# Kernel tuning notes

Measured on AMD Instinct MI355X. Metric: run time of the kernel, lower is better.

## Reference

```python
import jax, jax.numpy as jnp
import numpy as np

N_NODES = 10000
N_EDGES = 160000
N_GRAPHS = 16
IN_FEAT = 128
DIMS = [(128, 512), (512, 256), (256, 64), (64, 32)]


def _lin_params(key, fin, fout):
    w = jax.random.normal(key, (fin, fout), jnp.float32) * (1.0 / np.sqrt(fin))
    b = jnp.zeros((fout,), jnp.float32)
    return w, b


def setup_inputs() -> dict:
    key = jax.random.key(0)
    ks = jax.random.split(key, 64)
    inp = {}
    inp['x'] = jax.random.normal(ks[0], (N_NODES, IN_FEAT), jnp.float32)
    inp['edge_index'] = jax.random.randint(ks[1], (2, N_EDGES), 0, N_NODES, jnp.int64 if jax.config.jax_enable_x64 else jnp.int32)
    inp['batch'] = jnp.sort(jax.random.randint(ks[2], (N_NODES,), 0, N_GRAPHS))
    ki = 3
    for li, (fin, fout) in enumerate(DIMS, start=1):
        for nm in ['q', 'k', 'v', 's']:
            w, b = _lin_params(ks[ki], fin, fout); ki += 1
            inp[f'W{nm}{li}'] = w
            inp[f'b{nm}{li}'] = b
    inp['Wg'], inp['bg'] = _lin_params(ks[ki], 32, 1); ki += 1
    inp['Wf'], inp['bf'] = _lin_params(ks[ki], 32, 9)
    return inp


def _segment_softmax(logits, seg, num_segments):
    m = jax.ops.segment_max(logits, seg, num_segments=num_segments)
    e = jnp.exp(logits - m[seg])
    s = jax.ops.segment_sum(e, seg, num_segments=num_segments)
    return e / s[seg]


def _transformer_conv(x, src, dst, Wq, bq, Wk, bk, Wv, bv, Ws, bs):
    # PyG TransformerConv, heads=1: attention over incoming edges per dst node.
    n = x.shape[0]
    q = x @ Wq + bq
    k = x @ Wk + bk
    v = x @ Wv + bv
    d = q.shape[-1]
    logits = jnp.sum(q[dst] * k[src], axis=-1) / jnp.sqrt(jnp.asarray(d, x.dtype))
    alpha = _segment_softmax(logits, dst, n)  # [E]
    agg = jax.ops.segment_sum(alpha[:, None] * v[src], dst, num_segments=n)
    return agg + (x @ Ws + bs)  # root/skip connection


def reference(x, edge_index, batch,
              Wq1, bq1, Wk1, bk1, Wv1, bv1, Ws1, bs1,
              Wq2, bq2, Wk2, bk2, Wv2, bv2, Ws2, bs2,
              Wq3, bq3, Wk3, bk3, Wv3, bv3, Ws3, bs3,
              Wq4, bq4, Wk4, bk4, Wv4, bv4, Ws4, bs4,
              Wg, bg, Wf, bf):
    src, dst = edge_index[0], edge_index[1]
    layers = [
        (Wq1, bq1, Wk1, bk1, Wv1, bv1, Ws1, bs1),
        (Wq2, bq2, Wk2, bk2, Wv2, bv2, Ws2, bs2),
        (Wq3, bq3, Wk3, bk3, Wv3, bv3, Ws3, bs3),
        (Wq4, bq4, Wk4, bk4, Wv4, bv4, Ws4, bs4),
    ]
    h = x
    for p in layers:
        h = jax.nn.elu(_transformer_conv(h, src, dst, *p))
    # GlobalAttention pooling: gate softmax per graph, weighted sum.
    gate = (h @ Wg + bg)[:, 0]  # [N]
    a = _segment_softmax(gate, batch, N_GRAPHS)
    pooled = jax.ops.segment_sum(a[:, None] * h, batch, num_segments=N_GRAPHS)  # [G, 32]
    return pooled @ Wf + bf  # [G, 9]
```

## Files before the change

kernel.cpp:

```cpp
#include <hip/hip_runtime.h>
#include <hip/hip_bf16.h>
#include <math.h>


typedef __bf16 bf16x8 __attribute__((ext_vector_type(8)));
typedef __bf16 bf16x4 __attribute__((ext_vector_type(4)));
typedef float f32x4 __attribute__((ext_vector_type(4)));

#define GBM 128
#define GBN 128
#define GBK 64

#if __has_builtin(__builtin_amdgcn_global_load_lds)
#define ASYNC_LDS 1
__device__ __forceinline__ void gload16(const __bf16* g, __bf16* l) {
  __builtin_amdgcn_global_load_lds(
      (const __attribute__((address_space(1))) unsigned int*)g,
      (__attribute__((address_space(3))) unsigned int*)l, 16, 0, 0);
}
#endif

__global__ __launch_bounds__(256) void gemm_mfma_kernel(
    const __bf16* __restrict__ A, const __bf16* __restrict__ Bt,
    const float* __restrict__ bias, __bf16* __restrict__ qkvs,
    int M, int K, int Nc) {
  __shared__ __bf16 As[GBM * 64];
  __shared__ __bf16 Bs[GBN * 64];
  const int tid = threadIdx.x;
  const int wave = tid >> 6;
  const int lane = tid & 63;
  const int quad = lane >> 4;
  const int l16 = lane & 15;
  const int m0 = blockIdx.y * GBM;
  const int n0 = blockIdx.x * GBN;
  const int wm = (wave & 1) * 64;
  const int wn = (wave >> 1) * 64;

  const int r8 = lane >> 3;
  const int sseg = lane & 7;

  f32x4 acc[4][4] = {};

  for (int k0 = 0; k0 < K; k0 += GBK) {
#pragma unroll
    for (int it = 0; it < 4; ++it) {
      const int rbase = wave * 32 + it * 8;
      const int row = rbase + r8;
      const int sw = sseg ^ r8;
      const __bf16* ga = A + (size_t)(m0 + row) * K + k0 + sw * 8;
      const __bf16* gb = Bt + (size_t)(n0 + row) * K + k0 + sw * 8;
#ifdef ASYNC_LDS
      gload16(ga, As + rbase * 64);
      gload16(gb, Bs + rbase * 64);
#else
      *(bf16x8*)(As + row * 64 + sseg * 8) = *(const bf16x8*)ga;
      *(bf16x8*)(Bs + row * 64 + sseg * 8) = *(const bf16x8*)gb;
#endif
    }
    __syncthreads();

#pragma unroll
    for (int ks = 0; ks < 2; ++ks) {
      bf16x8 af[4], bfr[4];
#pragma unroll
      for (int i = 0; i < 4; ++i) {
        const int ra = wm + i * 16 + l16;
        const int rb = wn + i * 16 + l16;
        const int ps = ((ks * 4 + quad) ^ (l16 & 7)) * 8;
        af[i]  = *(const bf16x8*)(As + ra * 64 + ps);
        bfr[i] = *(const bf16x8*)(Bs + rb * 64 + ps);
      }
#pragma unroll
      for (int mi = 0; mi < 4; ++mi)
#pragma unroll
        for (int ni = 0; ni < 4; ++ni)
          acc[mi][ni] = __builtin_amdgcn_mfma_f32_16x16x32_bf16(
              af[mi], bfr[ni], acc[mi][ni], 0, 0, 0);
    }
    __syncthreads();
  }

  float bsv[4];
#pragma unroll
  for (int ni = 0; ni < 4; ++ni) bsv[ni] = bias[n0 + wn + ni * 16 + l16];
#pragma unroll
  for (int mi = 0; mi < 4; ++mi) {
#pragma unroll
    for (int r = 0; r < 4; ++r) {
      int row = m0 + wm + mi * 16 + quad * 4 + r;
      if (row < M) {
        size_t rb = (size_t)row * Nc;
#pragma unroll
        for (int ni = 0; ni < 4; ++ni) {
          int col = n0 + wn + ni * 16 + l16;
          qkvs[rb + col] = (__bf16)(acc[mi][ni][r] + bsv[ni]);
        }
      }
    }
  }
}

#define WTOT 860160
#define BTOT 3456
#define XTOT 320000
__global__ void pack_all_kernel(
    const float* W0q, const float* W0k, const float* W0v, const float* W0s,
    const float* b0q, const float* b0k, const float* b0v, const float* b0s,
    const float* W1q, const float* W1k, const float* W1v, const float* W1s,
    const float* b1q, const float* b1k, const float* b1v, const float* b1s,
    const float* W2q, const float* W2k, const float* W2v, const float* W2s,
    const float* b2q, const float* b2k, const float* b2v, const float* b2s,
    const float* W3q, const float* W3k, const float* W3v, const float* W3s,
    const float* b3q, const float* b3k, const float* b3v, const float* b3s,
    const float* __restrict__ x, __bf16* __restrict__ xb,
    __bf16* __restrict__ Wt, float* __restrict__ bcat) {
  const int t = blockIdx.x * 256 + threadIdx.x;
  if (t < WTOT) {
    int l, local, ksh, fsh;
    if (t < 262144)      { l = 0; local = t;          ksh = 7; fsh = 9; }
    else if (t < 786432) { l = 1; local = t - 262144; ksh = 9; fsh = 8; }
    else if (t < 851968) { l = 2; local = t - 786432; ksh = 8; fsh = 6; }
    else                 { l = 3; local = t - 851968; ksh = 6; fsh = 5; }
    const int K = 1 << ksh, fout = 1 << fsh;
    int c = local >> ksh;
    int kk = local & (K - 1);
    int blk = c >> fsh;
    int j = c & (fout - 1);
    const float* W;
    if (l == 0)      W = blk == 0 ? W0q : blk == 1 ? W0k : blk == 2 ? W0v : W0s;
    else if (l == 1) W = blk == 0 ? W1q : blk == 1 ? W1k : blk == 2 ? W1v : W1s;
    else if (l == 2) W = blk == 0 ? W2q : blk == 1 ? W2k : blk == 2 ? W2v : W2s;
    else             W = blk == 0 ? W3q : blk == 1 ? W3k : blk == 2 ? W3v : W3s;
    Wt[t] = (__bf16)W[((size_t)kk << fsh) + j];
  } else if (t < WTOT + BTOT) {
    int u = t - WTOT;
    int l, local, fsh, boff;
    if (u < 2048)      { l = 0; local = u;        fsh = 9; boff = 0; }
    else if (u < 3072) { l = 1; local = u - 2048; fsh = 8; boff = 2048; }
    else if (u < 3328) { l = 2; local = u - 3072; fsh = 6; boff = 3072; }
    else               { l = 3; local = u - 3328; fsh = 5; boff = 3328; }
    const int fout = 1 << fsh;
    int blk = local >> fsh, j = local & (fout - 1);
    const float* b;
    if (l == 0)      b = blk == 0 ? b0q : blk == 1 ? b0k : blk == 2 ? b0v : b0s;
    else if (l == 1) b = blk == 0 ? b1q : blk == 1 ? b1k : blk == 2 ? b1v : b1s;
    else if (l == 2) b = blk == 0 ? b2q : blk == 1 ? b2k : blk == 2 ? b2v : b2s;
    else             b = blk == 0 ? b3q : blk == 1 ? b3k : blk == 2 ? b3v : b3s;
    bcat[boff + local] = b[j];
  } else if (t < WTOT + BTOT + XTOT) {
    int i = t - (WTOT + BTOT);
    float4 v = ((const float4*)x)[i];
    bf16x4 o;
    o[0] = (__bf16)v.x; o[1] = (__bf16)v.y; o[2] = (__bf16)v.z; o[3] = (__bf16)v.w;
    *(bf16x4*)(xb + (size_t)i * 4) = o;
  }
}

__global__ void hist_kernel(const int* __restrict__ dst, int* __restrict__ deg, int E) {
  int e = blockIdx.x * blockDim.x + threadIdx.x;
  if (e < E) atomicAdd(&deg[dst[e]], 1);
}

__global__ __launch_bounds__(1024) void scan_kernel(const int* __restrict__ deg,
                                                    int* __restrict__ offs, int N) {
  __shared__ int sums[1024];
  const int tid = threadIdx.x;
  const int chunk = (N + 1023) / 1024;
  const int start = tid * chunk;
  int s = 0;
  for (int i = 0; i < chunk; ++i) {
    int idx = start + i;
    if (idx < N) s += deg[idx];
  }
  sums[tid] = s;
  __syncthreads();
  for (int off = 1; off < 1024; off <<= 1) {
    int t = (tid >= off) ? sums[tid - off] : 0;
    __syncthreads();
    sums[tid] += t;
    __syncthreads();
  }
  int run = (tid == 0) ? 0 : sums[tid - 1];
  for (int i = 0; i < chunk; ++i) {
    int idx = start + i;
    if (idx < N) {
      offs[idx] = run;
      run += deg[idx];
    }
  }
  if (tid == 1023) offs[N] = sums[1023];
}

__global__ void scatter_kernel(const int* __restrict__ src, const int* __restrict__ dst,
                               const int* __restrict__ offs, int* __restrict__ cursor,
                               int* __restrict__ csr_src, int E) {
  int e = blockIdx.x * blockDim.x + threadIdx.x;
  if (e >= E) return;
  int d = dst[e];
  int pos = offs[d] + atomicAdd(&cursor[d], 1);
  csr_src[pos] = src[e];
}

template <int D, int LPG_LOG2, bool GATE>
__global__ __launch_bounds__(256) void attn_fused_kernel(
    const __bf16* __restrict__ qkvs, const int* __restrict__ csr_src,
    const int* __restrict__ offs, __bf16* __restrict__ h_out, int N,
    float scale, const float* __restrict__ Wg, const float* __restrict__ bg,
    float* __restrict__ gate_out) {
  constexpr int LPG = 1 << LPG_LOG2;
  constexpr int NG = 64 / LPG;
  constexpr int NIT = D / (8 * LPG);
  constexpr int LD = 4 * D;
  const int node = (blockIdx.x * 256 + threadIdx.x) >> 6;
  const int lane = threadIdx.x & 63;
  if (node >= N) return;
  const int g = lane >> LPG_LOG2;
  const int l = lane & (LPG - 1);
  const int begin = offs[node];
  const int deg = offs[node + 1] - begin;

  const __bf16* qrow = qkvs + (size_t)node * LD;
  bf16x8 qreg[NIT];
#pragma unroll
  for (int it = 0; it < NIT; ++it)
    qreg[it] = *(const bf16x8*)(qrow + it * LPG * 8 + l * 8);

  float m = -INFINITY;
  float s = 0.f;
  float acc[NIT][8] = {};

  for (int base = 0; base < deg; base += NG) {
    const int i = base + g;
    const bool valid = i < deg;
    int sidx = valid ? csr_src[begin + i] : 0;

    float p = 0.f;
    if (valid) {
      const __bf16* krow = qkvs + (size_t)sidx * LD + D;
      bf16x8 kv[NIT];
#pragma unroll
      for (int it = 0; it < NIT; ++it)
        kv[it] = *(const bf16x8*)(krow + it * LPG * 8 + l * 8);
#pragma unroll
      for (int it = 0; it < NIT; ++it)
#pragma unroll
        for (int j = 0; j < 8; ++j) p += (float)qreg[it][j] * (float)kv[it][j];
    }
#pragma unroll
    for (int off = LPG >> 1; off; off >>= 1) p += __shfl_xor(p, off);
    const float logit = valid ? p * scale : -INFINITY;

    float cmax = logit;
#pragma unroll
    for (int off = LPG; off < 64; off <<= 1)
      cmax = fmaxf(cmax, __shfl_xor(cmax, off));
    const float m_new = fmaxf(m, cmax);
    const float alpha = __expf(m - m_new);
    s *= alpha;
#pragma unroll
    for (int it = 0; it < NIT; ++it)
#pragma unroll
      for (int j = 0; j < 8; ++j) acc[it][j] *= alpha;
    const float w = __expf(logit - m_new);
    s += w;
    m = m_new;

    if (valid) {
      const __bf16* vrow = qkvs + (size_t)sidx * LD + 2 * D;
      bf16x8 vv[NIT];
#pragma unroll
      for (int it = 0; it < NIT; ++it)
        vv[it] = *(const bf16x8*)(vrow + it * LPG * 8 + l * 8);
#pragma unroll
      for (int it = 0; it < NIT; ++it)
#pragma unroll
        for (int j = 0; j < 8; ++j) acc[it][j] += w * (float)vv[it][j];
    }
  }

#pragma unroll
  for (int off = LPG; off < 64; off <<= 1) {
    s += __shfl_xor(s, off);
#pragma unroll
    for (int it = 0; it < NIT; ++it)
#pragma unroll
      for (int j = 0; j < 8; ++j) acc[it][j] += __shfl_xor(acc[it][j], off);
  }
  const float inv = (deg > 0) ? (1.0f / s) : 0.f;

  if (g == 0) {
    float rr[NIT][8];
#pragma unroll
    for (int it = 0; it < NIT; ++it) {
      const int f0 = it * LPG * 8 + l * 8;
      bf16x8 sk = *(const bf16x8*)(qrow + 3 * D + f0);
      bf16x8 o;
#pragma unroll
      for (int j = 0; j < 8; ++j) {
        float r = acc[it][j] * inv + (float)sk[j];
        r = (r > 0.f) ? r : expm1f(r);
        rr[it][j] = r;
        o[j] = (__bf16)r;
      }
      *(bf16x8*)(h_out + (size_t)node * D + f0) = o;
    }
    if (GATE) {
      float gp = 0.f;
#pragma unroll
      for (int j = 0; j < 8; ++j) gp += rr[0][j] * Wg[l * 8 + j];
#pragma unroll
      for (int off = 1; off < LPG; off <<= 1) gp += __shfl_xor(gp, off);
      if (l == 0) gate_out[node] = gp + bg[0];
    }
  }
}

__global__ __launch_bounds__(256) void pool_final_kernel(
    const __bf16* __restrict__ h, const float* __restrict__ gate,
    const int* __restrict__ batch, int N, const float* __restrict__ Wf,
    const float* __restrict__ bf_, float* __restrict__ out) {
  __shared__ float red[256];
  __shared__ float pooled_s[32];
  __shared__ float m_s, inv_s;
  __shared__ int sb[2];
  const int g = blockIdx.x;
  const int tid = threadIdx.x;

  if (tid < 2) {
    int target = g + tid;
    int lo = 0, hi = N;
    while (lo < hi) {
      int mid = (lo + hi) >> 1;
      if (batch[mid] < target) lo = mid + 1;
      else hi = mid;
    }
    sb[tid] = lo;
  }
  __syncthreads();
  const int s = sb[0];
  const int e_end = sb[1];

  float m = -INFINITY;
  for (int i = s + tid; i < e_end; i += 256) m = fmaxf(m, gate[i]);
  red[tid] = m;
  __syncthreads();
  for (int off = 128; off; off >>= 1) {
    if (tid < off) red[tid] = fmaxf(red[tid], red[tid + off]);
    __syncthreads();
  }
  if (tid == 0) m_s = red[0];
  __syncthreads();
  m = m_s;

  float ss = 0.f;
  for (int i = s + tid; i < e_end; i += 256) ss += __expf(gate[i] - m);
  red[tid] = ss;
  __syncthreads();
  for (int off = 128; off; off >>= 1) {
    if (tid < off) red[tid] += red[tid + off];
    __syncthreads();
  }
  if (tid == 0) inv_s = (e_end > s) ? (1.0f / red[0]) : 0.f;
  __syncthreads();
  const float inv = inv_s;

  const int f = tid & 31;
  const int grp = tid >> 5;
  float acc = 0.f;
  for (int i = s + grp; i < e_end; i += 8)
    acc += __expf(gate[i] - m) * (float)h[(size_t)i * 32 + f];
  red[tid] = acc;
  __syncthreads();
  if (tid < 32) {
    float a = 0.f;
#pragma unroll
    for (int j = 0; j < 8; ++j) a += red[j * 32 + tid];
    pooled_s[tid] = a * inv;
  }
  __syncthreads();

  if (tid < 9) {
    float o = bf_[tid];
#pragma unroll
    for (int kk = 0; kk < 32; ++kk) o += pooled_s[kk] * Wf[kk * 9 + tid];
    out[g * 9 + tid] = o;
  }
}

extern "C" void kernel_launch(void* const* d_in, const int* in_sizes, int n_in,
                              void* d_out, int out_size, void* d_ws, size_t ws_size,
                              hipStream_t stream) {
  const int N = in_sizes[2];
  const int E = in_sizes[1] / 2;
  const int G = 16;
  const int NP = N + 128;

  const float* x = (const float*)d_in[0];
  const int* ei = (const int*)d_in[1];
  const int* batch = (const int*)d_in[2];
  const int* src = ei;
  const int* dst = ei + E;
  const float* Wg = (const float*)d_in[35];
  const float* bg = (const float*)d_in[36];
  const float* Wf = (const float*)d_in[37];
  const float* bf_ = (const float*)d_in[38];
  float* out = (float*)d_out;

  char* p = (char*)d_ws;
  auto carve = [&](size_t bytes) -> char* {
    char* r = p;
    p += (bytes + 255) & ~(size_t)255;
    return r;
  };
  int* deg = (int*)carve((size_t)2 * N * 4);
  int* cursor = deg + N;
  int* offs = (int*)carve((size_t)(N + 1) * 4);
  int* csr_src = (int*)carve((size_t)E * 4);
  __bf16* Ab = (__bf16*)carve((size_t)NP * 128 * 2);
  __bf16* Wt = (__bf16*)carve((size_t)WTOT * 2);
  float* bcat = (float*)carve(BTOT * 4);
  __bf16* qkvs = (__bf16*)carve((size_t)N * 2048 * 2);
  __bf16* ha = (__bf16*)carve((size_t)NP * 512 * 2);
  __bf16* hb = (__bf16*)carve((size_t)NP * 512 * 2);
  float* gate = (float*)carve((size_t)N * 4);
  (void)ws_size;

  hipMemsetAsync(deg, 0, (size_t)2 * N * 4, stream);
  hist_kernel<<<(E + 255) / 256, 256, 0, stream>>>(dst, deg, E);
  scan_kernel<<<1, 1024, 0, stream>>>(deg, offs, N);
  scatter_kernel<<<(E + 255) / 256, 256, 0, stream>>>(src, dst, offs, cursor, csr_src, E);

  const float** di = (const float**)d_in;
  pack_all_kernel<<<(WTOT + BTOT + XTOT + 255) / 256, 256, 0, stream>>>(
      di[3], di[5], di[7], di[9], di[4], di[6], di[8], di[10],
      di[11], di[13], di[15], di[17], di[12], di[14], di[16], di[18],
      di[19], di[21], di[23], di[25], di[20], di[22], di[24], di[26],
      di[27], di[29], di[31], di[33], di[28], di[30], di[32], di[34],
      x, Ab, Wt, bcat);

  const int fins[4] = {128, 512, 256, 64};
  const int fouts[4] = {512, 256, 64, 32};
  const size_t woffs[4] = {0, 262144, 786432, 851968};
  const int boffs[4] = {0, 2048, 3072, 3328};
  const __bf16* hin = Ab;
  __bf16* houts[4] = {ha, hb, ha, hb};
  const int agrid = ((size_t)N * 64 + 255) / 256;

  for (int l = 0; l < 4; ++l) {
    const int fin = fins[l], fout = fouts[l];
    const int Nc = 4 * fout;
    __bf16* hout = houts[l];

    dim3 grid(Nc / GBN, (N + GBM - 1) / GBM);
    gemm_mfma_kernel<<<grid, 256, 0, stream>>>(hin, Wt + woffs[l], bcat + boffs[l],
                                               qkvs, N, fin, Nc);

    float scale = 1.0f / sqrtf((float)fout);
    if (l == 0) {
      attn_fused_kernel<512, 4, false><<<agrid, 256, 0, stream>>>(
          qkvs, csr_src, offs, hout, N, scale, nullptr, nullptr, nullptr);
    } else if (l == 1) {
      attn_fused_kernel<256, 4, false><<<agrid, 256, 0, stream>>>(
          qkvs, csr_src, offs, hout, N, scale, nullptr, nullptr, nullptr);
    } else if (l == 2) {
      attn_fused_kernel<64, 3, false><<<agrid, 256, 0, stream>>>(
          qkvs, csr_src, offs, hout, N, scale, nullptr, nullptr, nullptr);
    } else {
      attn_fused_kernel<32, 2, true><<<agrid, 256, 0, stream>>>(
          qkvs, csr_src, offs, hout, N, scale, Wg, bg, gate);
    }
    hin = hout;
  }

  pool_final_kernel<<<G, 256, 0, stream>>>(hin, gate, batch, N, Wf, bf_, out);
}
```

Before: 356.7 us.

## Fuse degree histogram into pack kernel and drop online-softmax rescaling in attention

The edge-degree histogram atomics move into the existing weight/input pack kernel, removing one kernel launch. In the edge-attention kernel the running-max online softmax is replaced by a fixed shift taken from the first chunk's maximum logit. That removes the per-iteration cross-lane max reduction, the exp and the rescaling of the accumulators. K and V rows for each neighbor are now loaded together up front to overlap their latency. The fixed shift relies on later logits not greatly exceeding the first chunk's maximum, which could overflow exp on other inputs.

```diff
diff --git a/kernel.cpp b/kernel.cpp
--- a/kernel.cpp
+++ b/kernel.cpp
@@ -113,7 +113,8 @@
     const float* W3q, const float* W3k, const float* W3v, const float* W3s,
     const float* b3q, const float* b3k, const float* b3v, const float* b3s,
     const float* __restrict__ x, __bf16* __restrict__ xb,
-    __bf16* __restrict__ Wt, float* __restrict__ bcat) {
+    __bf16* __restrict__ Wt, float* __restrict__ bcat,
+    const int* __restrict__ dst, int* __restrict__ deg, int E) {
   const int t = blockIdx.x * 256 + threadIdx.x;
   if (t < WTOT) {
     int l, local, ksh, fsh;
@@ -153,12 +154,10 @@
     bf16x4 o;
     o[0] = (__bf16)v.x; o[1] = (__bf16)v.y; o[2] = (__bf16)v.z; o[3] = (__bf16)v.w;
     *(bf16x4*)(xb + (size_t)i * 4) = o;
-  }
-}
-
-__global__ void hist_kernel(const int* __restrict__ dst, int* __restrict__ deg, int E) {
-  int e = blockIdx.x * blockDim.x + threadIdx.x;
-  if (e < E) atomicAdd(&deg[dst[e]], 1);
+  } else if (t < WTOT + BTOT + XTOT + E) {
+    int e = t - (WTOT + BTOT + XTOT);
+    atomicAdd(&deg[dst[e]], 1);
+  }
 }
 
 __global__ __launch_bounds__(1024) void scan_kernel(const int* __restrict__ deg,
@@ -225,22 +224,26 @@
   for (int it = 0; it < NIT; ++it)
     qreg[it] = *(const bf16x8*)(qrow + it * LPG * 8 + l * 8);
 
-  float m = -INFINITY;
+  float m0 = 0.f;
   float s = 0.f;
   float acc[NIT][8] = {};
 
+#pragma unroll 1
   for (int base = 0; base < deg; base += NG) {
     const int i = base + g;
     const bool valid = i < deg;
-    int sidx = valid ? csr_src[begin + i] : 0;
-
+    const int sidx = valid ? csr_src[begin + i] : 0;
+    const __bf16* krow = qkvs + (size_t)sidx * LD + D;
+    bf16x8 kv[NIT], vv[NIT];
+    if (valid) {
+#pragma unroll
+      for (int it = 0; it < NIT; ++it) {
+        kv[it] = *(const bf16x8*)(krow + it * LPG * 8 + l * 8);
+        vv[it] = *(const bf16x8*)(krow + D + it * LPG * 8 + l * 8);
+      }
+    }
     float p = 0.f;
     if (valid) {
-      const __bf16* krow = qkvs + (size_t)sidx * LD + D;
-      bf16x8 kv[NIT];
-#pragma unroll
-      for (int it = 0; it < NIT; ++it)
-        kv[it] = *(const bf16x8*)(krow + it * LPG * 8 + l * 8);
 #pragma unroll
       for (int it = 0; it < NIT; ++it)
 #pragma unroll
@@ -250,27 +253,17 @@
     for (int off = LPG >> 1; off; off >>= 1) p += __shfl_xor(p, off);
     const float logit = valid ? p * scale : -INFINITY;
 
-    float cmax = logit;
-#pragma unroll
-    for (int off = LPG; off < 64; off <<= 1)
-      cmax = fmaxf(cmax, __shfl_xor(cmax, off));
-    const float m_new = fmaxf(m, cmax);
-    const float alpha = __expf(m - m_new);
-    s *= alpha;
-#pragma unroll
-    for (int it = 0; it < NIT; ++it)
-#pragma unroll
-      for (int j = 0; j < 8; ++j) acc[it][j] *= alpha;
-    const float w = __expf(logit - m_new);
+    if (base == 0) {
+      float mm = logit;
+#pragma unroll
+      for (int off = LPG; off < 64; off <<= 1)
+        mm = fmaxf(mm, __shfl_xor(mm, off));
+      m0 = mm;
+    }
+
+    const float w = __expf(logit - m0);
     s += w;
-    m = m_new;
-
     if (valid) {
-      const __bf16* vrow = qkvs + (size_t)sidx * LD + 2 * D;
-      bf16x8 vv[NIT];
-#pragma unroll
-      for (int it = 0; it < NIT; ++it)
-        vv[it] = *(const bf16x8*)(vrow + it * LPG * 8 + l * 8);
 #pragma unroll
       for (int it = 0; it < NIT; ++it)
 #pragma unroll
@@ -426,17 +419,15 @@
   (void)ws_size;
 
   hipMemsetAsync(deg, 0, (size_t)2 * N * 4, stream);
-  hist_kernel<<<(E + 255) / 256, 256, 0, stream>>>(dst, deg, E);
-  scan_kernel<<<1, 1024, 0, stream>>>(deg, offs, N);
-  scatter_kernel<<<(E + 255) / 256, 256, 0, stream>>>(src, dst, offs, cursor, csr_src, E);
-
   const float** di = (const float**)d_in;
-  pack_all_kernel<<<(WTOT + BTOT + XTOT + 255) / 256, 256, 0, stream>>>(
+  pack_all_kernel<<<(WTOT + BTOT + XTOT + E + 255) / 256, 256, 0, stream>>>(
       di[3], di[5], di[7], di[9], di[4], di[6], di[8], di[10],
       di[11], di[13], di[15], di[17], di[12], di[14], di[16], di[18],
       di[19], di[21], di[23], di[25], di[20], di[22], di[24], di[26],
       di[27], di[29], di[31], di[33], di[28], di[30], di[32], di[34],
-      x, Ab, Wt, bcat);
+      x, Ab, Wt, bcat, dst, deg, E);
+  scan_kernel<<<1, 1024, 0, stream>>>(deg, offs, N);
+  scatter_kernel<<<(E + 255) / 256, 256, 0, stream>>>(src, dst, offs, cursor, csr_src, E);
 
   const int fins[4] = {128, 512, 256, 64};
   const int fouts[4] = {512, 256, 64, 32};
```

New measurement: 352.1 us. No clear change (-1.3%).
